# Performance work log

Measured on AMD Instinct MI355X. Metric: run time of the kernel, lower is better.

The kernel has to match this reference:

```python
import jax, jax.numpy as jnp
import numpy as np

B, DIN, H, DOUT, NC = 1024, 343, 512, 311, 4


def cubic(y0, y1, y2, y3, mu):
    # Catmull-Rom cubic interpolation (matches PFNN.cubic)
    return ((-0.5 * y0 + 1.5 * y1 - 1.5 * y2 + 0.5 * y3) * mu * mu * mu
            + (y0 - 2.5 * y1 + 2.0 * y2 - 0.5 * y3) * mu * mu
            + (-0.5 * y0 + 0.5 * y2) * mu + y1)


def setup_inputs() -> dict:
    key = jax.random.key(0)
    ks = jax.random.split(key, 7)
    s = 0.05
    x = jax.random.uniform(ks[0], (B, DIN), dtype=jnp.float32)  # phase = x[:, -1] in [0,1)
    W0 = jax.random.normal(ks[1], (NC, H, DIN - 1), dtype=jnp.float32) * s
    W1 = jax.random.normal(ks[2], (NC, H, H), dtype=jnp.float32) * s
    W2 = jax.random.normal(ks[3], (NC, DOUT, H), dtype=jnp.float32) * s
    b0 = jax.random.normal(ks[4], (NC, H), dtype=jnp.float32) * s
    b1 = jax.random.normal(ks[5], (NC, H), dtype=jnp.float32) * s
    b2 = jax.random.normal(ks[6], (NC, DOUT), dtype=jnp.float32) * s
    return {"x": x, "W0": W0, "W1": W1, "W2": W2, "b0": b0, "b1": b1, "b2": b2}


def reference(x, W0, W1, W2, b0, b1, b2):
    nc = W0.shape[0]
    phase = x[:, -1]                       # [B]
    pscale = nc * phase
    mu = jnp.mod(pscale, 1.0)              # [B]
    k1 = jnp.mod(pscale.astype(jnp.int32), nc)
    k0 = jnp.mod(k1 - 1, nc)
    k2 = jnp.mod(k1 + 1, nc)
    k3 = jnp.mod(k1 + 2, nc)
    muW = mu[:, None, None]
    mub = mu[:, None]

    def interp(P, m):
        return cubic(P[k0], P[k1], P[k2], P[k3], m)

    W0i = interp(W0, muW)  # [B, 512, DIN-1]
    W1i = interp(W1, muW)  # [B, 512, 512]
    W2i = interp(W2, muW)  # [B, DOUT, 512]
    b0i = interp(b0, mub)
    b1i = interp(b1, mub)
    b2i = interp(b2, mub)

    h0 = x[:, :-1]                                              # [B, DIN-1]
    h1 = jax.nn.elu(jnp.einsum('boi,bi->bo', W0i, h0) + b0i)    # [B, 512]
    h2 = jax.nn.elu(jnp.einsum('boi,bi->bo', W1i, h1) + b1i)    # [B, 512]
    h3 = jnp.einsum('boi,bi->bo', W2i, h2) + b2i                # [B, DOUT]
    return h3
```

## Files before the change

### kernel.cpp

```cpp
#include <hip/hip_runtime.h>
#include <math.h>

typedef short bf16x8 __attribute__((ext_vector_type(8)));
typedef float f32x16 __attribute__((ext_vector_type(16)));

__device__ __forceinline__ unsigned short f2bf(float f) {
    union { float f; unsigned u; } x; x.f = f;
    unsigned r = x.u + 0x7FFFu + ((x.u >> 16) & 1u);
    return (unsigned short)(r >> 16);
}

template<int NKS_T>
__device__ void transpose_tile(const float* __restrict__ W, const float* __restrict__ bias,
                               int rowbase, int rowlimit, int Kreal, int ldsrc,
                               unsigned short* __restrict__ dst, float* s, int tid)
{
    constexpr int NCHK = NKS_T / 4;
    const int r = tid >> 3, l = tid & 7;
    const int ks_l = tid >> 6, lane = tid & 63;
    const int m = lane & 31, h = lane >> 5;
    for (int kc = 0; kc < NCHK; ++kc) {
        {
            int kb = kc * 64 + l * 8;
            const bool rv = r < rowlimit;
            const float* src = W + (size_t)(rowbase + r) * ldsrc + kb;
            float v[8];
            if (rv && kb + 7 < Kreal) {
                #pragma unroll
                for (int i = 0; i < 8; ++i) v[i] = src[i];
            } else {
                #pragma unroll
                for (int i = 0; i < 8; ++i) {
                    int k = kb + i;
                    v[i] = (rv && k < Kreal) ? src[i]
                         : ((rv && k == Kreal) ? (bias ? bias[rowbase + r] : 1.0f) : 0.f);
                }
            }
            #pragma unroll
            for (int i = 0; i < 8; ++i) s[r * 66 + l * 8 + i] = v[i];
        }
        __syncthreads();
        {
            bf16x8 pk;
            #pragma unroll
            for (int j = 0; j < 8; ++j)
                pk[j] = (short)f2bf(s[m * 66 + ks_l * 16 + h * 8 + j]);
            *(bf16x8*)(dst + ((size_t)(kc * 4 + ks_l) * 64 + lane) * 8) = pk;
        }
        __syncthreads();
    }
}

__global__ void __launch_bounds__(256) phaseA_kernel(
    const float* __restrict__ x,
    const float* __restrict__ W0, const float* __restrict__ W1, const float* __restrict__ W2,
    const float* __restrict__ bias0, const float* __restrict__ bias1, const float* __restrict__ bias2,
    float* __restrict__ coef, unsigned short* __restrict__ xf,
    unsigned short* __restrict__ H1f, unsigned short* __restrict__ H2f,
    unsigned short* __restrict__ Wf0, unsigned short* __restrict__ Wf1, unsigned short* __restrict__ Wf2)
{
    __shared__ float s[32 * 66];
    const int bid = blockIdx.x, tid = threadIdx.x;

    if (bid < 32) {
        const int bt = bid;
        if (tid < 32) {
            int b = bt * 32 + tid;
            float phase = x[(size_t)b * 343 + 342];
            float ps = 4.0f * phase;
            int k1 = (int)ps;
            float mu = ps - (float)k1;
            k1 &= 3;
            float mu2 = mu * mu, mu3 = mu2 * mu;
            float c0 = -0.5f * mu3 +        mu2 - 0.5f * mu;
            float c1 =  1.5f * mu3 - 2.5f * mu2 + 1.0f;
            float c2 = -1.5f * mu3 + 2.0f * mu2 + 0.5f * mu;
            float c3 =  0.5f * mu3 - 0.5f * mu2;
            float cc[4];
            cc[(k1 + 3) & 3] = c0;
            cc[k1]           = c1;
            cc[(k1 + 1) & 3] = c2;
            cc[(k1 + 2) & 3] = c3;
            *(float4*)(coef + b * 4) = make_float4(cc[0], cc[1], cc[2], cc[3]);
        }
        {
            int kk = tid >> 6, lane = tid & 63;
            size_t off = ((size_t)(bt * 36 + 32 + kk) * 64 + lane) * 8;
            bf16x8 v;
            #pragma unroll
            for (int j = 0; j < 8; ++j)
                v[j] = (short)((kk == 0 && (lane >> 5) == 0 && j == 0) ? 0x3F80 : 0);
            *(bf16x8*)(H1f + off) = v;
            *(bf16x8*)(H2f + off) = v;
        }
        transpose_tile<24>(x, nullptr, bt * 32, 32, 342, 343,
                           xf + (size_t)bt * 24 * 512, s, tid);
    } else if (bid < 96) {
        int idx = bid - 32, n = idx >> 4, ot = idx & 15;
        transpose_tile<24>(W0, bias0, n * 512 + ot * 32, 32, 342, 342,
                           Wf0 + (size_t)(n * 16 + ot) * 24 * 512, s, tid);
    } else if (bid < 160) {
        int idx = bid - 96, n = idx >> 4, ot = idx & 15;
        transpose_tile<36>(W1, bias1, n * 512 + ot * 32, 32, 512, 512,
                           Wf1 + (size_t)(n * 16 + ot) * 36 * 512, s, tid);
    } else {
        int idx = bid - 160, n = idx / 10, ot = idx % 10;
        int rl = 311 - ot * 32; if (rl > 32) rl = 32;
        transpose_tile<36>(W2, bias2, n * 311 + ot * 32, rl, 512, 512,
                           Wf2 + (size_t)(n * 10 + ot) * 36 * 512, s, tid);
    }
}

template<bool ELU, bool OUT_BF16, int KP, int OPAD>
__device__ __forceinline__ void layer_phase(
    const unsigned short* __restrict__ Wf,
    const unsigned short* __restrict__ Hf,
    const float* __restrict__ coef,
    unsigned short* __restrict__ HoutF,
    float* __restrict__ outF, int Oreal,
    float* red, int bid, int tid)
{
    constexpr int NOT = OPAD / 32, NKS = KP / 16, KSQ = NKS / 4;
    constexpr int CH = 3, NC2 = KSQ / CH;
    const int lane = tid & 63, w = tid >> 6;
    const int m = lane & 31, h = lane >> 5;
    const size_t nstr = (size_t)NOT * NKS * 512;

    const int ot = bid >> 5, bt = bid & 31;
    const unsigned short* wbase = Wf + ((size_t)ot * NKS + w * KSQ) * 512 + (size_t)lane * 8;
    const unsigned short* bbase = Hf + ((size_t)bt * NKS + w * KSQ) * 512 + (size_t)lane * 8;

    f32x16 acc0 = {}, acc1 = {}, acc2 = {}, acc3 = {};
    bf16x8 Ab[2][CH][4], Bb[2][CH];

    #pragma unroll
    for (int sI = 0; sI < CH; ++sI) {
        Bb[0][sI] = *(const bf16x8*)(bbase + (size_t)sI * 512);
        #pragma unroll
        for (int n = 0; n < 4; ++n)
            Ab[0][sI][n] = *(const bf16x8*)(wbase + (size_t)n * nstr + (size_t)sI * 512);
    }
    #pragma unroll
    for (int c = 0; c < NC2; ++c) {
        const int cur = c & 1;
        if (c + 1 < NC2) {
            const int nxt = cur ^ 1;
            #pragma unroll
            for (int sI = 0; sI < CH; ++sI) {
                int st = (c + 1) * CH + sI;
                Bb[nxt][sI] = *(const bf16x8*)(bbase + (size_t)st * 512);
                #pragma unroll
                for (int n = 0; n < 4; ++n)
                    Ab[nxt][sI][n] = *(const bf16x8*)(wbase + (size_t)n * nstr + (size_t)st * 512);
            }
        }
        #pragma unroll
        for (int sI = 0; sI < CH; ++sI) {
            acc0 = __builtin_amdgcn_mfma_f32_32x32x16_bf16(Ab[cur][sI][0], Bb[cur][sI], acc0, 0, 0, 0);
            acc1 = __builtin_amdgcn_mfma_f32_32x32x16_bf16(Ab[cur][sI][1], Bb[cur][sI], acc1, 0, 0, 0);
            acc2 = __builtin_amdgcn_mfma_f32_32x32x16_bf16(Ab[cur][sI][2], Bb[cur][sI], acc2, 0, 0, 0);
            acc3 = __builtin_amdgcn_mfma_f32_32x32x16_bf16(Ab[cur][sI][3], Bb[cur][sI], acc3, 0, 0, 0);
        }
    }

    const int b = bt * 32 + m;
    float4 cf = *(const float4*)(coef + b * 4);
    #pragma unroll
    for (int g = 0; g < 4; ++g)
        #pragma unroll
        for (int j = 0; j < 4; ++j) {
            int rI = g * 4 + j;
            float v = cf.x * acc0[rI] + cf.y * acc1[rI] + cf.z * acc2[rI] + cf.w * acc3[rI];
            red[w * 1024 + (8 * g + 4 * h + j) * 32 + m] = v;
        }
    __syncthreads();
    {
        float vv[4];
        #pragma unroll
        for (int j = 0; j < 4; ++j) {
            int row = 8 * w + 4 * h + j;
            float v = red[row * 32 + m] + red[1024 + row * 32 + m]
                    + red[2048 + row * 32 + m] + red[3072 + row * 32 + m];
            if (ELU) v = (v > 0.f) ? v : expm1f(v);
            vv[j] = v;
        }
        if (OUT_BF16) {
            size_t off = (((size_t)bt * 36 + ot * 2 + (w >> 1)) * 64
                          + (w & 1) * 32 + m) * 8 + 4 * h;
            ushort4 pk;
            pk.x = f2bf(vv[0]); pk.y = f2bf(vv[1]); pk.z = f2bf(vv[2]); pk.w = f2bf(vv[3]);
            *(ushort4*)(HoutF + off) = pk;
        } else {
            int orow = ot * 32 + 8 * w + 4 * h;
            #pragma unroll
            for (int j = 0; j < 4; ++j)
                if (orow + j < Oreal) outF[(size_t)b * Oreal + orow + j] = vv[j];
        }
    }
}

__global__ void __launch_bounds__(256, 2) layer0_kernel(
    const unsigned short* __restrict__ Wf0, const unsigned short* __restrict__ xf,
    const float* __restrict__ coef, unsigned short* __restrict__ H1f)
{
    __shared__ float red[4 * 1024];
    layer_phase<true, true, 384, 512>(Wf0, xf, coef, H1f, nullptr, 512,
                                      red, blockIdx.x, threadIdx.x);
}
__global__ void __launch_bounds__(256, 2) layer1_kernel(
    const unsigned short* __restrict__ Wf1, const unsigned short* __restrict__ H1f,
    const float* __restrict__ coef, unsigned short* __restrict__ H2f)
{
    __shared__ float red[4 * 1024];
    layer_phase<true, true, 576, 512>(Wf1, H1f, coef, H2f, nullptr, 512,
                                      red, blockIdx.x, threadIdx.x);
}
__global__ void __launch_bounds__(256, 2) layer2_kernel(
    const unsigned short* __restrict__ Wf2, const unsigned short* __restrict__ H2f,
    const float* __restrict__ coef, float* __restrict__ outF)
{
    __shared__ float red[4 * 1024];
    layer_phase<false, false, 576, 320>(Wf2, H2f, coef, nullptr, outF, 311,
                                        red, blockIdx.x, threadIdx.x);
}

extern "C" void kernel_launch(void* const* d_in, const int* in_sizes, int n_in,
                              void* d_out, int out_size, void* d_ws, size_t ws_size,
                              hipStream_t stream) {
    (void)in_sizes; (void)n_in; (void)out_size; (void)ws_size;
    const float* x  = (const float*)d_in[0];
    const float* W0 = (const float*)d_in[1];
    const float* W1 = (const float*)d_in[2];
    const float* W2 = (const float*)d_in[3];
    const float* b0 = (const float*)d_in[4];
    const float* b1 = (const float*)d_in[5];
    const float* b2 = (const float*)d_in[6];
    float* out = (float*)d_out;

    char* wsb = (char*)d_ws;
    float*          coef = (float*)(wsb + 0);
    unsigned short* xf   = (unsigned short*)(wsb + 16384);
    unsigned short* H1f  = (unsigned short*)(wsb + 802816);
    unsigned short* H2f  = (unsigned short*)(wsb + 1982464);
    unsigned short* Wf0  = (unsigned short*)(wsb + 3162112);
    unsigned short* Wf1  = (unsigned short*)(wsb + 4734976);
    unsigned short* Wf2  = (unsigned short*)(wsb + 7094272);

    phaseA_kernel<<<dim3(200), dim3(256), 0, stream>>>(
        x, W0, W1, W2, b0, b1, b2, coef, xf, H1f, H2f, Wf0, Wf1, Wf2);
    layer0_kernel<<<dim3(512), dim3(256), 0, stream>>>(Wf0, xf,  coef, H1f);
    layer1_kernel<<<dim3(512), dim3(256), 0, stream>>>(Wf1, H1f, coef, H2f);
    layer2_kernel<<<dim3(320), dim3(256), 0, stream>>>(Wf2, H2f, coef, out);
}
```

Before: 95.26 us.

## Fuse prep and three layer kernels into one cooperative kernel with grid syncs

Replaces four separate launches (weight/input transpose prep plus three layer GEMMs) with a single cooperative kernel that uses grid.sync between phases. The prep work is also split into finer per-chunk work items spread over all 512 blocks instead of 200 blocks each looping over chunks. This is meant to remove launch gaps and tail effects between kernels and to parallelise the prep phase more evenly. In exchange it depends on all 512 blocks being co-resident (2 per CU), adds grid-wide barrier costs, and idles blocks 320-511 during the last layer.

Result: slower. 286.8 us (+201.0%).

```diff
diff --git a/kernel.cpp b/kernel.cpp
--- a/kernel.cpp
+++ b/kernel.cpp
@@ -1,5 +1,8 @@
 #include <hip/hip_runtime.h>
+#include <hip/hip_cooperative_groups.h>
 #include <math.h>
+
+namespace cg = cooperative_groups;
 
 typedef short bf16x8 __attribute__((ext_vector_type(8)));
 typedef float f32x16 __attribute__((ext_vector_type(16)));
@@ -10,57 +13,145 @@
     return (unsigned short)(r >> 16);
 }
 
-template<int NKS_T>
-__device__ void transpose_tile(const float* __restrict__ W, const float* __restrict__ bias,
-                               int rowbase, int rowlimit, int Kreal, int ldsrc,
-                               unsigned short* __restrict__ dst, float* s, int tid)
+__device__ __forceinline__ void do_chunk(
+    const float* __restrict__ W, const float* __restrict__ bias,
+    int rowbase, int rowlimit, int Kreal, int ldsrc,
+    unsigned short* __restrict__ dst, int kc, float* s, int tid)
 {
-    constexpr int NCHK = NKS_T / 4;
     const int r = tid >> 3, l = tid & 7;
     const int ks_l = tid >> 6, lane = tid & 63;
     const int m = lane & 31, h = lane >> 5;
-    for (int kc = 0; kc < NCHK; ++kc) {
-        {
-            int kb = kc * 64 + l * 8;
-            const bool rv = r < rowlimit;
-            const float* src = W + (size_t)(rowbase + r) * ldsrc + kb;
-            float v[8];
-            if (rv && kb + 7 < Kreal) {
+    {
+        int kb = kc * 64 + l * 8;
+        const bool rv = r < rowlimit;
+        const float* src = W + (size_t)(rowbase + r) * ldsrc + kb;
+        float v[8];
+        if (rv && kb + 7 < Kreal) {
+            #pragma unroll
+            for (int i = 0; i < 8; ++i) v[i] = src[i];
+        } else {
+            #pragma unroll
+            for (int i = 0; i < 8; ++i) {
+                int k = kb + i;
+                v[i] = (rv && k < Kreal) ? src[i]
+                     : ((rv && k == Kreal) ? (bias ? bias[rowbase + r] : 1.0f) : 0.f);
+            }
+        }
+        #pragma unroll
+        for (int i = 0; i < 8; ++i) s[r * 66 + l * 8 + i] = v[i];
+    }
+    __syncthreads();
+    {
+        bf16x8 pk;
+        #pragma unroll
+        for (int j = 0; j < 8; ++j)
+            pk[j] = (short)f2bf(s[m * 66 + ks_l * 16 + h * 8 + j]);
+        *(bf16x8*)(dst + ((size_t)(kc * 4 + ks_l) * 64 + lane) * 8) = pk;
+    }
+    __syncthreads();
+}
+
+template<bool ELU, bool OUT_BF16, int KP, int OPAD>
+__device__ __forceinline__ void layer_phase(
+    const unsigned short* __restrict__ Wf,
+    const unsigned short* __restrict__ Hf,
+    const float* __restrict__ coef,
+    unsigned short* __restrict__ HoutF,
+    float* __restrict__ outF, int Oreal,
+    float* red, int bid, int tid)
+{
+    constexpr int NOT = OPAD / 32, NKS = KP / 16, KSQ = NKS / 4;
+    constexpr int CH = 3, NC2 = KSQ / CH;
+    const int lane = tid & 63, w = tid >> 6;
+    const int m = lane & 31, h = lane >> 5;
+    const size_t nstr = (size_t)NOT * NKS * 512;
+
+    const int ot = bid >> 5, bt = bid & 31;
+    const unsigned short* wbase = Wf + ((size_t)ot * NKS + w * KSQ) * 512 + (size_t)lane * 8;
+    const unsigned short* bbase = Hf + ((size_t)bt * NKS + w * KSQ) * 512 + (size_t)lane * 8;
+
+    f32x16 acc0 = {}, acc1 = {}, acc2 = {}, acc3 = {};
+    bf16x8 Ab[2][CH][4], Bb[2][CH];
+
+    #pragma unroll
+    for (int sI = 0; sI < CH; ++sI) {
+        Bb[0][sI] = *(const bf16x8*)(bbase + (size_t)sI * 512);
+        #pragma unroll
+        for (int n = 0; n < 4; ++n)
+            Ab[0][sI][n] = *(const bf16x8*)(wbase + (size_t)n * nstr + (size_t)sI * 512);
+    }
+    #pragma unroll
+    for (int c = 0; c < NC2; ++c) {
+        const int cur = c & 1;
+        if (c + 1 < NC2) {
+            const int nxt = cur ^ 1;
+            #pragma unroll
+            for (int sI = 0; sI < CH; ++sI) {
+                int st = (c + 1) * CH + sI;
+                Bb[nxt][sI] = *(const bf16x8*)(bbase + (size_t)st * 512);
                 #pragma unroll
-                for (int i = 0; i < 8; ++i) v[i] = src[i];
-            } else {
-                #pragma unroll
-                for (int i = 0; i < 8; ++i) {
-                    int k = kb + i;
-                    v[i] = (rv && k < Kreal) ? src[i]
-                         : ((rv && k == Kreal) ? (bias ? bias[rowbase + r] : 1.0f) : 0.f);
-                }
+                for (int n = 0; n < 4; ++n)
+                    Ab[nxt][sI][n] = *(const bf16x8*)(wbase + (size_t)n * nstr + (size_t)st * 512);
             }
-            #pragma unroll
-            for (int i = 0; i < 8; ++i) s[r * 66 + l * 8 + i] = v[i];
-        }
-        __syncthreads();
-        {
-            bf16x8 pk;
-            #pragma unroll
-            for (int j = 0; j < 8; ++j)
-                pk[j] = (short)f2bf(s[m * 66 + ks_l * 16 + h * 8 + j]);
-            *(bf16x8*)(dst + ((size_t)(kc * 4 + ks_l) * 64 + lane) * 8) = pk;
-        }
-        __syncthreads();
-    }
-}
-
-__global__ void __launch_bounds__(256) phaseA_kernel(
+        }
+        #pragma unroll
+        for (int sI = 0; sI < CH; ++sI) {
+            acc0 = __builtin_amdgcn_mfma_f32_32x32x16_bf16(Ab[cur][sI][0], Bb[cur][sI], acc0, 0, 0, 0);
+            acc1 = __builtin_amdgcn_mfma_f32_32x32x16_bf16(Ab[cur][sI][1], Bb[cur][sI], acc1, 0, 0, 0);
+            acc2 = __builtin_amdgcn_mfma_f32_32x32x16_bf16(Ab[cur][sI][2], Bb[cur][sI], acc2, 0, 0, 0);
+            acc3 = __builtin_amdgcn_mfma_f32_32x32x16_bf16(Ab[cur][sI][3], Bb[cur][sI], acc3, 0, 0, 0);
+        }
+    }
+
+    const int b = bt * 32 + m;
+    float4 cf = *(const float4*)(coef + b * 4);
+    #pragma unroll
+    for (int g = 0; g < 4; ++g)
+        #pragma unroll
+        for (int j = 0; j < 4; ++j) {
+            int rI = g * 4 + j;
+            float v = cf.x * acc0[rI] + cf.y * acc1[rI] + cf.z * acc2[rI] + cf.w * acc3[rI];
+            red[w * 1024 + (8 * g + 4 * h + j) * 32 + m] = v;
+        }
+    __syncthreads();
+    {
+        float vv[4];
+        #pragma unroll
+        for (int j = 0; j < 4; ++j) {
+            int row = 8 * w + 4 * h + j;
+            float v = red[row * 32 + m] + red[1024 + row * 32 + m]
+                    + red[2048 + row * 32 + m] + red[3072 + row * 32 + m];
+            if (ELU) v = (v > 0.f) ? v : expm1f(v);
+            vv[j] = v;
+        }
+        if (OUT_BF16) {
+            size_t off = (((size_t)bt * 36 + ot * 2 + (w >> 1)) * 64
+                          + (w & 1) * 32 + m) * 8 + 4 * h;
+            ushort4 pk;
+            pk.x = f2bf(vv[0]); pk.y = f2bf(vv[1]); pk.z = f2bf(vv[2]); pk.w = f2bf(vv[3]);
+            *(ushort4*)(HoutF + off) = pk;
+        } else {
+            int orow = ot * 32 + 8 * w + 4 * h;
+            #pragma unroll
+            for (int j = 0; j < 4; ++j)
+                if (orow + j < Oreal) outF[(size_t)b * Oreal + orow + j] = vv[j];
+        }
+    }
+    __syncthreads();
+}
+
+__global__ void __launch_bounds__(256, 2) fused_kernel(
     const float* __restrict__ x,
     const float* __restrict__ W0, const float* __restrict__ W1, const float* __restrict__ W2,
     const float* __restrict__ bias0, const float* __restrict__ bias1, const float* __restrict__ bias2,
     float* __restrict__ coef, unsigned short* __restrict__ xf,
     unsigned short* __restrict__ H1f, unsigned short* __restrict__ H2f,
-    unsigned short* __restrict__ Wf0, unsigned short* __restrict__ Wf1, unsigned short* __restrict__ Wf2)
+    unsigned short* __restrict__ Wf0, unsigned short* __restrict__ Wf1, unsigned short* __restrict__ Wf2,
+    float* __restrict__ outF)
 {
-    __shared__ float s[32 * 66];
+    __shared__ float sm[4096];
     const int bid = blockIdx.x, tid = threadIdx.x;
+    cg::grid_group grid = cg::this_grid();
 
     if (bid < 32) {
         const int bt = bid;
@@ -93,135 +184,36 @@
             *(bf16x8*)(H1f + off) = v;
             *(bf16x8*)(H2f + off) = v;
         }
-        transpose_tile<24>(x, nullptr, bt * 32, 32, 342, 343,
-                           xf + (size_t)bt * 24 * 512, s, tid);
-    } else if (bid < 96) {
-        int idx = bid - 32, n = idx >> 4, ot = idx & 15;
-        transpose_tile<24>(W0, bias0, n * 512 + ot * 32, 32, 342, 342,
-                           Wf0 + (size_t)(n * 16 + ot) * 24 * 512, s, tid);
-    } else if (bid < 160) {
-        int idx = bid - 96, n = idx >> 4, ot = idx & 15;
-        transpose_tile<36>(W1, bias1, n * 512 + ot * 32, 32, 512, 512,
-                           Wf1 + (size_t)(n * 16 + ot) * 36 * 512, s, tid);
-    } else {
-        int idx = bid - 160, n = idx / 10, ot = idx % 10;
-        int rl = 311 - ot * 32; if (rl > 32) rl = 32;
-        transpose_tile<36>(W2, bias2, n * 311 + ot * 32, rl, 512, 512,
-                           Wf2 + (size_t)(n * 10 + ot) * 36 * 512, s, tid);
-    }
-}
-
-template<bool ELU, bool OUT_BF16, int KP, int OPAD>
-__device__ __forceinline__ void layer_phase(
-    const unsigned short* __restrict__ Wf,
-    const unsigned short* __restrict__ Hf,
-    const float* __restrict__ coef,
-    unsigned short* __restrict__ HoutF,
-    float* __restrict__ outF, int Oreal,
-    float* red, int bid, int tid)
-{
-    constexpr int NOT = OPAD / 32, NKS = KP / 16, KSQ = NKS / 4;
-    constexpr int CH = 3, NC2 = KSQ / CH;
-    const int lane = tid & 63, w = tid >> 6;
-    const int m = lane & 31, h = lane >> 5;
-    const size_t nstr = (size_t)NOT * NKS * 512;
-
-    const int ot = bid >> 5, bt = bid & 31;
-    const unsigned short* wbase = Wf + ((size_t)ot * NKS + w * KSQ) * 512 + (size_t)lane * 8;
-    const unsigned short* bbase = Hf + ((size_t)bt * NKS + w * KSQ) * 512 + (size_t)lane * 8;
-
-    f32x16 acc0 = {}, acc1 = {}, acc2 = {}, acc3 = {};
-    bf16x8 Ab[2][CH][4], Bb[2][CH];
-
-    #pragma unroll
-    for (int sI = 0; sI < CH; ++sI) {
-        Bb[0][sI] = *(const bf16x8*)(bbase + (size_t)sI * 512);
-        #pragma unroll
-        for (int n = 0; n < 4; ++n)
-            Ab[0][sI][n] = *(const bf16x8*)(wbase + (size_t)n * nstr + (size_t)sI * 512);
-    }
-    #pragma unroll
-    for (int c = 0; c < NC2; ++c) {
-        const int cur = c & 1;
-        if (c + 1 < NC2) {
-            const int nxt = cur ^ 1;
-            #pragma unroll
-            for (int sI = 0; sI < CH; ++sI) {
-                int st = (c + 1) * CH + sI;
-                Bb[nxt][sI] = *(const bf16x8*)(bbase + (size_t)st * 512);
-                #pragma unroll
-                for (int n = 0; n < 4; ++n)
-                    Ab[nxt][sI][n] = *(const bf16x8*)(wbase + (size_t)n * nstr + (size_t)st * 512);
-            }
-        }
-        #pragma unroll
-        for (int sI = 0; sI < CH; ++sI) {
-            acc0 = __builtin_amdgcn_mfma_f32_32x32x16_bf16(Ab[cur][sI][0], Bb[cur][sI], acc0, 0, 0, 0);
-            acc1 = __builtin_amdgcn_mfma_f32_32x32x16_bf16(Ab[cur][sI][1], Bb[cur][sI], acc1, 0, 0, 0);
-            acc2 = __builtin_amdgcn_mfma_f32_32x32x16_bf16(Ab[cur][sI][2], Bb[cur][sI], acc2, 0, 0, 0);
-            acc3 = __builtin_amdgcn_mfma_f32_32x32x16_bf16(Ab[cur][sI][3], Bb[cur][sI], acc3, 0, 0, 0);
-        }
-    }
-
-    const int b = bt * 32 + m;
-    float4 cf = *(const float4*)(coef + b * 4);
-    #pragma unroll
-    for (int g = 0; g < 4; ++g)
-        #pragma unroll
-        for (int j = 0; j < 4; ++j) {
-            int rI = g * 4 + j;
-            float v = cf.x * acc0[rI] + cf.y * acc1[rI] + cf.z * acc2[rI] + cf.w * acc3[rI];
-            red[w * 1024 + (8 * g + 4 * h + j) * 32 + m] = v;
-        }
-    __syncthreads();
-    {
-        float vv[4];
-        #pragma unroll
-        for (int j = 0; j < 4; ++j) {
-            int row = 8 * w + 4 * h + j;
-            float v = red[row * 32 + m] + red[1024 + row * 32 + m]
-                    + red[2048 + row * 32 + m] + red[3072 + row * 32 + m];
-            if (ELU) v = (v > 0.f) ? v : expm1f(v);
-            vv[j] = v;
-        }
-        if (OUT_BF16) {
-            size_t off = (((size_t)bt * 36 + ot * 2 + (w >> 1)) * 64
-                          + (w & 1) * 32 + m) * 8 + 4 * h;
-            ushort4 pk;
-            pk.x = f2bf(vv[0]); pk.y = f2bf(vv[1]); pk.z = f2bf(vv[2]); pk.w = f2bf(vv[3]);
-            *(ushort4*)(HoutF + off) = pk;
+    }
+
+    for (int j = bid; j < 1512; j += 512) {
+        if (j < 192) {
+            int bt = j / 6, kc = j % 6;
+            do_chunk(x, nullptr, bt * 32, 32, 342, 343,
+                     xf + (size_t)bt * 24 * 512, kc, sm, tid);
+        } else if (j < 576) {
+            int t = j - 192, tile = t / 6, kc = t % 6, n = tile >> 4, ot = tile & 15;
+            do_chunk(W0, bias0, n * 512 + ot * 32, 32, 342, 342,
+                     Wf0 + (size_t)(n * 16 + ot) * 24 * 512, kc, sm, tid);
+        } else if (j < 1152) {
+            int t = j - 576, tile = t / 9, kc = t % 9, n = tile >> 4, ot = tile & 15;
+            do_chunk(W1, bias1, n * 512 + ot * 32, 32, 512, 512,
+                     Wf1 + (size_t)(n * 16 + ot) * 36 * 512, kc, sm, tid);
         } else {
-            int orow = ot * 32 + 8 * w + 4 * h;
-            #pragma unroll
-            for (int j = 0; j < 4; ++j)
-                if (orow + j < Oreal) outF[(size_t)b * Oreal + orow + j] = vv[j];
-        }
-    }
-}
-
-__global__ void __launch_bounds__(256, 2) layer0_kernel(
-    const unsigned short* __restrict__ Wf0, const unsigned short* __restrict__ xf,
-    const float* __restrict__ coef, unsigned short* __restrict__ H1f)
-{
-    __shared__ float red[4 * 1024];
-    layer_phase<true, true, 384, 512>(Wf0, xf, coef, H1f, nullptr, 512,
-                                      red, blockIdx.x, threadIdx.x);
-}
-__global__ void __launch_bounds__(256, 2) layer1_kernel(
-    const unsigned short* __restrict__ Wf1, const unsigned short* __restrict__ H1f,
-    const float* __restrict__ coef, unsigned short* __restrict__ H2f)
-{
-    __shared__ float red[4 * 1024];
-    layer_phase<true, true, 576, 512>(Wf1, H1f, coef, H2f, nullptr, 512,
-                                      red, blockIdx.x, threadIdx.x);
-}
-__global__ void __launch_bounds__(256, 2) layer2_kernel(
-    const unsigned short* __restrict__ Wf2, const unsigned short* __restrict__ H2f,
-    const float* __restrict__ coef, float* __restrict__ outF)
-{
-    __shared__ float red[4 * 1024];
-    layer_phase<false, false, 576, 320>(Wf2, H2f, coef, nullptr, outF, 311,
-                                        red, blockIdx.x, threadIdx.x);
+            int t = j - 1152, tile = t / 9, kc = t % 9, n = tile / 10, ot = tile % 10;
+            int rl = 311 - ot * 32; if (rl > 32) rl = 32;
+            do_chunk(W2, bias2, n * 311 + ot * 32, rl, 512, 512,
+                     Wf2 + (size_t)(n * 10 + ot) * 36 * 512, kc, sm, tid);
+        }
+    }
+
+    grid.sync();
+    layer_phase<true,  true,  384, 512>(Wf0, xf,  coef, H1f, nullptr, 512, sm, bid, tid);
+    grid.sync();
+    layer_phase<true,  true,  576, 512>(Wf1, H1f, coef, H2f, nullptr, 512, sm, bid, tid);
+    grid.sync();
+    if (bid < 320)
+        layer_phase<false, false, 576, 320>(Wf2, H2f, coef, nullptr, outF, 311, sm, bid, tid);
 }
 
 extern "C" void kernel_launch(void* const* d_in, const int* in_sizes, int n_in,
@@ -246,9 +238,10 @@
     unsigned short* Wf1  = (unsigned short*)(wsb + 4734976);
     unsigned short* Wf2  = (unsigned short*)(wsb + 7094272);
 
-    phaseA_kernel<<<dim3(200), dim3(256), 0, stream>>>(
-        x, W0, W1, W2, b0, b1, b2, coef, xf, H1f, H2f, Wf0, Wf1, Wf2);
-    layer0_kernel<<<dim3(512), dim3(256), 0, stream>>>(Wf0, xf,  coef, H1f);
-    layer1_kernel<<<dim3(512), dim3(256), 0, stream>>>(Wf1, H1f, coef, H2f);
-    layer2_kernel<<<dim3(320), dim3(256), 0, stream>>>(Wf2, H2f, coef, out);
-}
+    void* args[] = { (void*)&x, (void*)&W0, (void*)&W1, (void*)&W2,
+                     (void*)&b0, (void*)&b1, (void*)&b2,
+                     (void*)&coef, (void*)&xf, (void*)&H1f, (void*)&H2f,
+                     (void*)&Wf0, (void*)&Wf1, (void*)&Wf2, (void*)&out };
+    hipLaunchCooperativeKernel((const void*)fused_kernel, dim3(512), dim3(256),
+                               args, 0, stream);
+}
```
